# Kernel optimization log

Hardware: AMD Instinct MI355X
Metric: run time of the kernel (lower is better)

## Reference

```python
import jax, jax.numpy as jnp
import numpy as np

N_TOKEN = 267735
CUTOFFS = [20000, 40000, 200000, 267735]
ENDS = [0] + CUTOFFS
CLUSTER_DIMS = [1024, 256, 64, 16]   # d_embed // div_val**i
CLUSTER_SIZES = [20000, 20000, 160000, 67735]
D_PROJ = 1024
T, B = 256, 4
N_CLUSTERS = 3


def setup_inputs() -> dict:
    key = jax.random.key(0)
    ks = jax.random.split(key, 16)
    inp = {}
    inp["hidden"] = jax.random.normal(ks[0], (T, B, D_PROJ), jnp.float32)
    inp["target"] = jax.random.randint(ks[1], (T, B), 0, N_TOKEN)
    for i in range(4):
        inp[f"W{i}"] = jax.random.normal(ks[2 + 3 * i], (CLUSTER_SIZES[i], CLUSTER_DIMS[i]), jnp.float32) * 0.02
        inp[f"b{i}"] = jnp.zeros((CLUSTER_SIZES[i],), jnp.float32)
        inp[f"P{i}"] = jax.random.normal(ks[3 + 3 * i], (CLUSTER_DIMS[i], D_PROJ), jnp.float32) * 0.02
    inp["cluster_weight"] = jax.random.normal(ks[14], (N_CLUSTERS, 1024), jnp.float32) * 0.02
    inp["cluster_bias"] = jnp.zeros((N_CLUSTERS,), jnp.float32)
    return inp


def _logit(x, W, b, P):
    # x: [T,B,d_proj], P: [e,d_proj], W: [n,e] -> [T,B,n]
    y = jnp.einsum('ibd,ed->ibe', x, P)
    return jnp.einsum('ibe,ne->ibn', y, W) + b


def _gather(logprob, tgt):
    # pick logprob[t, b, tgt[t,b]]
    return jnp.take_along_axis(logprob, tgt[..., None], axis=-1)[..., 0]


def reference(hidden, target, W0, b0, P0, W1, b1, P1, W2, b2, P2, W3, b3, P3,
              cluster_weight, cluster_bias):
    Ws = [W0, W1, W2, W3]
    bs = [b0, b1, b2, b3]
    Ps = [P0, P1, P2, P3]
    loss = jnp.zeros(target.shape, jnp.float32)
    head_logprob = None
    for i in range(4):
        l_idx, r_idx = ENDS[i], ENDS[i + 1]
        mask = (target >= l_idx) & (target < r_idx)
        cur_t = jnp.maximum(jnp.minimum(target, r_idx - 1) - l_idx, 0)
        if i == 0:
            Wh = jnp.concatenate([W0, cluster_weight], axis=0)
            bh = jnp.concatenate([b0, cluster_bias], axis=0)
            head_logprob = jax.nn.log_softmax(_logit(hidden, Wh, bh, P0), axis=-1)
            cur_loss = _gather(head_logprob, cur_t)
        else:
            tail_logprob = jax.nn.log_softmax(_logit(hidden, Ws[i], bs[i], Ps[i]), axis=-1)
            logprob_i = head_logprob[..., CUTOFFS[0] + i - 1, None] + tail_logprob
            cur_loss = _gather(logprob_i, cur_t)
        loss = jnp.where(mask, cur_loss, loss)
    return jnp.mean(-loss)
```

## Files before the change

### kernel.cpp

```cpp
#include <hip/hip_runtime.h>
#include <math.h>

typedef short short8 __attribute__((ext_vector_type(8)));
typedef float f32x4 __attribute__((ext_vector_type(4)));
typedef unsigned long long u64;

#define LOG2E 1.4426950408889634f

__device__ __forceinline__ unsigned short f2bf_rne(float f) {
    unsigned u = __float_as_uint(f);
    unsigned r = (u + 0x7fff + ((u >> 16) & 1)) >> 16;
    return (unsigned short)r;
}
__device__ __forceinline__ float bf2f(unsigned short h) {
    return __uint_as_float(((unsigned)h) << 16);
}
__device__ __forceinline__ void load_lds16(const void* g, void* l) {
    __builtin_amdgcn_global_load_lds((const __attribute__((address_space(1))) void*)g,
                                     (__attribute__((address_space(3))) void*)l,
                                     16, 0, 0);
}
template<int N>
__device__ __forceinline__ void waitvm() {
    asm volatile("s_waitcnt vmcnt(%0)" :: "n"(N) : "memory");
}
__device__ __forceinline__ u64 pack8_fp8(const float* v, float s) {
    int lo = 0, hi = 0;
    lo = __builtin_amdgcn_cvt_pk_fp8_f32(v[0] * s, v[1] * s, lo, false);
    lo = __builtin_amdgcn_cvt_pk_fp8_f32(v[2] * s, v[3] * s, lo, true);
    hi = __builtin_amdgcn_cvt_pk_fp8_f32(v[4] * s, v[5] * s, hi, false);
    hi = __builtin_amdgcn_cvt_pk_fp8_f32(v[6] * s, v[7] * s, hi, true);
    return (u64)(unsigned)lo | ((u64)(unsigned)hi << 32);
}

__global__ void cvt_h(const float* __restrict__ in, unsigned short* __restrict__ out)
{
    const int i = blockIdx.x * 256 + threadIdx.x;
    const float4 v = *(const float4*)(in + (size_t)i * 4);
    ushort4 h;
    h.x = f2bf_rne(v.x); h.y = f2bf_rne(v.y);
    h.z = f2bf_rne(v.z); h.w = f2bf_rne(v.w);
    *(ushort4*)(out + (size_t)i * 4) = h;
}

struct ProjDesc {
    const float* B;
    unsigned short* Cbf;
    unsigned char* Cf8;
    int ldc; int nreal; int N; int Kpad; int gy_begin;
};

__global__ __launch_bounds__(256) void prepproj(
    const unsigned short* __restrict__ A,
    ProjDesc p0, ProjDesc p1, ProjDesc p2, ProjDesc p3,
    const float* __restrict__ W0, const float* __restrict__ cw,
    const float* __restrict__ W1, const float* __restrict__ W2,
    const float* __restrict__ W3,
    const float* __restrict__ b0, const float* __restrict__ cb,
    const float* __restrict__ b1, const float* __restrict__ b2,
    const float* __restrict__ b3,
    unsigned char* __restrict__ Wb0, unsigned char* __restrict__ Wb1,
    unsigned char* __restrict__ Wb2, unsigned char* __restrict__ Wb3,
    float* __restrict__ bp)
{
    __shared__ char smem[34816];

    const int tid = threadIdx.x;
    const int bx = blockIdx.x;

    if (bx >= 96) {
        const unsigned E0 = 1286144u;
        const unsigned E1 = 1613824u;
        const unsigned E2 = 2260992u;
        const unsigned E3 = 2539520u;
        const unsigned E4 = 2607520u;
        const unsigned stride = (gridDim.x - 96) * 256u;
        for (unsigned u = (bx - 96) * 256u + tid; u < E4; u += stride) {
            if (u < E3) {
                const float* src = nullptr;
                unsigned char* dstm; unsigned tile, kg2, r, tstride;
                if (u < E0) {
                    tile = u >> 13; const unsigned rem = u & 8191u;
                    kg2 = rem >> 7; r = rem & 127u;
                    const unsigned row = tile * 128u + r;
                    if (row < 20000u)      src = W0 + (size_t)row * 1024 + kg2 * 16;
                    else if (row < 20003u) src = cw + (size_t)(row - 20000u) * 1024 + kg2 * 16;
                    dstm = Wb0; tstride = 131072u;
                } else if (u < E1) {
                    const unsigned j = u - E0;
                    tile = j >> 11; const unsigned rem = j & 2047u;
                    kg2 = rem >> 7; r = rem & 127u;
                    const unsigned row = tile * 128u + r;
                    if (row < 20000u) src = W1 + (size_t)row * 256 + kg2 * 16;
                    dstm = Wb1; tstride = 32768u;
                } else if (u < E2) {
                    const unsigned j = u - E1;
                    tile = j >> 9; kg2 = (j >> 7) & 3u; r = j & 127u;
                    const unsigned row = tile * 128u + r;
                    if (row < 160000u) src = W2 + (size_t)row * 64 + kg2 * 16;
                    dstm = Wb2; tstride = 8192u;
                } else {
                    const unsigned j = u - E2;
                    tile = j >> 9; kg2 = (j >> 7) & 3u; r = j & 127u;
                    const unsigned row = tile * 128u + r;
                    if (kg2 == 0 && row < 67735u) src = W3 + (size_t)row * 16;
                    dstm = Wb3; tstride = 8192u;
                }
                float f[16];
                if (src) {
#pragma unroll
                    for (int q = 0; q < 4; ++q) {
                        const float4 v = *(const float4*)(src + q * 4);
                        f[q * 4 + 0] = v.x; f[q * 4 + 1] = v.y;
                        f[q * 4 + 2] = v.z; f[q * 4 + 3] = v.w;
                    }
                } else {
#pragma unroll
                    for (int q = 0; q < 16; ++q) f[q] = 0.f;
                }
                u64* dst = (u64*)(dstm + (size_t)tile * tstride);
                dst[(2 * kg2) * 128 + r]     = pack8_fp8(f,     16.0f);
                dst[(2 * kg2 + 1) * 128 + r] = pack8_fp8(f + 8, 16.0f);
            } else {
                const unsigned idx0 = (u - E3) * 4u;
                float e[4];
#pragma unroll
                for (int j = 0; j < 4; ++j) {
                    const unsigned idx = idx0 + j;
                    float v;
                    if (idx < 20096u) {
                        v = (idx < 20000u) ? b0[idx] * LOG2E
                          : (idx < 20003u) ? cb[idx - 20000u] * LOG2E : -1e30f;
                    } else if (idx < 40576u) {
                        const unsigned i1 = idx - 20096u;
                        v = (i1 < 20000u) ? b1[i1] * LOG2E : -1e30f;
                    } else if (idx < 202368u) {
                        const unsigned i2 = idx - 40576u;
                        v = (i2 < 160000u) ? b2[i2] * LOG2E : -1e30f;
                    } else {
                        const unsigned i3 = idx - 202368u;
                        v = (i3 < 67735u) ? b3[i3] * LOG2E : -1e30f;
                    }
                    e[j] = v;
                }
                *(float4*)(bp + idx0) = make_float4(e[0], e[1], e[2], e[3]);
            }
        }
        return;
    }

    unsigned short* As = (unsigned short*)smem;
    unsigned short* Bs = (unsigned short*)(smem + 16384);

    const int mt = bx & 7;
    const int py = bx >> 3;
    ProjDesc p = (py >= p3.gy_begin) ? p3 : (py >= p2.gy_begin) ? p2
               : (py >= p1.gy_begin) ? p1 : p0;

    const int w = tid >> 6;
    const int l = tid & 63;
    const int m0 = mt * 128;
    const int n0 = (py - p.gy_begin) * 128;
    const int wm = (w >> 1) * 64;
    const int wn = (w & 1) * 64;
    const int lane16 = l & 15;
    const int quad = l >> 4;

    const unsigned short* aptr[4];
    int ag_base[4];
#pragma unroll
    for (int i = 0; i < 4; ++i) {
        const int g = w * 256 + i * 64 + l;
        aptr[i] = A + (size_t)(m0 + (g & 127)) * 1024 + (g >> 7) * 8;
        ag_base[i] = (w * 256 + i * 64) * 8;
    }

    const int bn = tid >> 1;
    const int bhalf = tid & 1;
    int brow = n0 + bn;
    if (brow > p.N - 1) brow = p.N - 1;
    const float* brow_ptr = p.B + (size_t)brow * 1024;

    f32x4 acc[4][4] = {};

    for (int k0 = 0; k0 < 1024; k0 += 64) {
        __syncthreads();
#pragma unroll
        for (int i = 0; i < 4; ++i)
            load_lds16(aptr[i] + k0, (void*)&As[ag_base[i]]);
#pragma unroll
        for (int j = 0; j < 8; ++j) {
            const int kq = bhalf * 8 + j;
            const float4 v = *(const float4*)(brow_ptr + k0 + kq * 4);
            const unsigned px = __builtin_amdgcn_perm(__float_as_uint(v.y), __float_as_uint(v.x), 0x07060302);
            const unsigned pyv = __builtin_amdgcn_perm(__float_as_uint(v.w), __float_as_uint(v.z), 0x07060302);
            const int gran = (kq >> 1) * 128 + bn;
            *(uint2*)&Bs[gran * 8 + (kq & 1) * 4] = make_uint2(px, pyv);
        }
        __syncthreads();

#pragma unroll
        for (int kk = 0; kk < 2; ++kk) {
            const int kgb = kk * 4 + quad;
            short8 af[4], bfr[4];
#pragma unroll
            for (int mi = 0; mi < 4; ++mi)
                af[mi] = *(const short8*)&As[(kgb * 128 + wm + mi * 16 + lane16) * 8];
#pragma unroll
            for (int ni = 0; ni < 4; ++ni)
                bfr[ni] = *(const short8*)&Bs[(kgb * 128 + wn + ni * 16 + lane16) * 8];
#pragma unroll
            for (int mi = 0; mi < 4; ++mi)
#pragma unroll
                for (int ni = 0; ni < 4; ++ni)
                    acc[mi][ni] = __builtin_amdgcn_mfma_f32_16x16x32_bf16(
                        af[mi], bfr[ni], acc[mi][ni], 0, 0, 0);
        }
    }

#pragma unroll
    for (int mi = 0; mi < 4; ++mi)
#pragma unroll
        for (int ni = 0; ni < 4; ++ni) {
            const int n = n0 + wn + ni * 16 + lane16;
            if (n < p.ldc) {
#pragma unroll
                for (int r = 0; r < 4; ++r) {
                    const int m = m0 + wm + mi * 16 + quad * 4 + r;
                    const float v = (n < p.nreal) ? acc[mi][ni][r] : 0.f;
                    p.Cbf[(size_t)m * p.ldc + n] = f2bf_rne(v);
                }
            }
        }

    float* bounce = (float*)smem;
    u64* Yout = (u64*)p.Cf8 + (size_t)mt * 16 * p.Kpad;
    for (int c = 0; c < 2; ++c) {
        const int colbase = n0 + c * 64;
        if (colbase >= p.Kpad) break;
        __syncthreads();
        if ((w & 1) == c) {
#pragma unroll
            for (int mi = 0; mi < 4; ++mi)
#pragma unroll
                for (int ni = 0; ni < 4; ++ni) {
                    const int ncol = ni * 16 + lane16;
                    const bool real = (colbase + ncol) < p.nreal;
#pragma unroll
                    for (int r = 0; r < 4; ++r) {
                        const int m = wm + mi * 16 + quad * 4 + r;
                        bounce[m * 66 + ncol] = real ? acc[mi][ni][r] : 0.f;
                    }
                }
        }
        __syncthreads();
#pragma unroll
        for (int i = 0; i < 4; ++i) {
            const int g = i * 256 + tid;
            const int kgl = g >> 7;
            const int m = g & 127;
            float v[8];
#pragma unroll
            for (int j = 0; j < 8; ++j) v[j] = bounce[m * 66 + kgl * 8 + j];
            Yout[((colbase >> 3) + kgl) * 128 + m] = pack8_fp8(v, 4.0f);
        }
    }
}

struct ExpDesc {
    const unsigned char* A;
    const unsigned char* W;
    const float* bias;
    float* part;
    int Kpad; int ksl; int kmask; int gy_begin; int slab;
};

__global__ __launch_bounds__(512) void exp_gemm(ExpDesc d0, ExpDesc d1, ExpDesc d2, ExpDesc d3)
{
    __shared__ u64 As[2][2048];
    __shared__ u64 Bs[2][1024];
    __shared__ float biasLds[2][128];

    const int p = blockIdx.x;
    const int gy = blockIdx.y;

    ExpDesc d = (gy >= d3.gy_begin) ? d3 : (gy >= d2.gy_begin) ? d2
              : (gy >= d1.gy_begin) ? d1 : d0;

    const int tid = threadIdx.x;
    const int w = tid >> 6;
    const int l = tid & 63;
    const int wmt = w >> 2;
    const int wq = w & 3;
    const int wm = (wq >> 1) * 64;
    const int wn = (wq & 1) * 64;
    const int lane16 = l & 15;
    const int quad = l >> 4;

    const int tiles_begin = (gy - d.gy_begin) * d.slab;
    const int T = d.slab << d.ksl;
    const int kmask = d.kmask;
    const int ksl = d.ksl;
    const bool haveA = (kmask != 0);

    const size_t tstride = (size_t)128 * d.Kpad;
    const unsigned char* Abase0 = d.A + (size_t)p * tstride;
    const unsigned char* Abase1 = d.A + (size_t)(p + 4) * tstride;
    const unsigned char* Bbase = d.W + (size_t)tiles_begin * tstride;
    const float* biasBase = d.bias + (size_t)tiles_begin * 128;

    const int so = tid * 16;
    const int bu = (w * 4 + l) * 16;

    if (haveA) {
        load_lds16(Abase0 + so, (char*)As[0] + so);
        load_lds16(Abase1 + so, (char*)As[0] + 8192 + so);
        load_lds16(Bbase + so, (char*)Bs[0] + so);
        if (l < 4) load_lds16(biasBase + (bu >> 2), (char*)biasLds + bu);
        load_lds16(Abase0 + 8192 + so, (char*)As[1] + so);
        load_lds16(Abase1 + 8192 + so, (char*)As[1] + 8192 + so);
        load_lds16(Bbase + 8192 + so, (char*)Bs[1] + so);
        if (l < 4) load_lds16(biasBase + (bu >> 2), (char*)biasLds + 512 + bu);
    } else {
        load_lds16(Abase0 + so, (char*)As[0] + so);
        load_lds16(Abase1 + so, (char*)As[0] + 8192 + so);
        load_lds16(Bbase + so, (char*)Bs[0] + so);
        if (l < 4) load_lds16(biasBase + (bu >> 2), (char*)biasLds + bu);
        load_lds16(Bbase + tstride + so, (char*)Bs[1] + so);
        if (l < 4) load_lds16(biasBase + 128 + (bu >> 2), (char*)biasLds + 512 + bu);
    }

    f32x4 acc[4][4] = {};
    float rowsum[4][4] = {};
    const float c1 = LOG2E / 64.0f;

    for (int it = 0; it < T; ++it) {
        const int slot = it & 1;
        if (it + 1 < T) { if (haveA) waitvm<4>(); else waitvm<2>(); }
        else            { waitvm<0>(); }
        __builtin_amdgcn_s_barrier();
        __builtin_amdgcn_sched_barrier(0);

        const u64* Ar = (haveA ? As[slot] : As[0]) + wmt * 1024;
        const u64* Br = Bs[slot];
#pragma unroll
        for (int ks = 0; ks < 2; ++ks) {
            u64 af[4], bfr[4];
#pragma unroll
            for (int mi = 0; mi < 4; ++mi)
                af[mi] = Ar[(ks * 4 + quad) * 128 + wm + mi * 16 + lane16];
#pragma unroll
            for (int ni = 0; ni < 4; ++ni)
                bfr[ni] = Br[(ks * 4 + quad) * 128 + wn + ni * 16 + lane16];
#pragma unroll
            for (int mi = 0; mi < 4; ++mi)
#pragma unroll
                for (int ni = 0; ni < 4; ++ni)
                    acc[mi][ni] = __builtin_amdgcn_mfma_f32_16x16x32_fp8_fp8(
                        (long)af[mi], (long)bfr[ni], acc[mi][ni], 0, 0, 0);
        }

        const bool doflush = ((it & kmask) == kmask);
        float biasc[4];
        if (doflush) {
#pragma unroll
            for (int ni = 0; ni < 4; ++ni)
                biasc[ni] = biasLds[slot][wn + ni * 16 + lane16];
            asm volatile("s_waitcnt lgkmcnt(0)" ::: "memory");
        }

        __builtin_amdgcn_sched_barrier(0);
        __builtin_amdgcn_s_barrier();

        if (it + 2 < T) {
            const int nit = it + 2;
            const int kc = nit & kmask;
            const int tile = nit >> ksl;
            if (haveA) {
                load_lds16(Abase0 + kc * 8192 + so, (char*)As[slot] + so);
                load_lds16(Abase1 + kc * 8192 + so, (char*)As[slot] + 8192 + so);
            }
            const unsigned char* bc = Bbase + (size_t)tile * tstride + kc * 8192;
            load_lds16(bc + so, (char*)Bs[slot] + so);
            if (l < 4)
                load_lds16(biasBase + (size_t)tile * 128 + (bu >> 2),
                           (char*)biasLds + slot * 512 + bu);
        }

        if (doflush) {
#pragma unroll
            for (int mi = 0; mi < 4; ++mi)
#pragma unroll
                for (int r = 0; r < 4; ++r) {
                    float s = exp2f(fmaf(acc[mi][0][r], c1, biasc[0]))
                            + exp2f(fmaf(acc[mi][1][r], c1, biasc[1]))
                            + exp2f(fmaf(acc[mi][2][r], c1, biasc[2]))
                            + exp2f(fmaf(acc[mi][3][r], c1, biasc[3]));
                    rowsum[mi][r] += s;
                }
#pragma unroll
            for (int mi = 0; mi < 4; ++mi)
#pragma unroll
                for (int ni = 0; ni < 4; ++ni)
                    acc[mi][ni] = (f32x4){0.f, 0.f, 0.f, 0.f};
        }
    }

#pragma unroll
    for (int off = 1; off < 16; off <<= 1)
#pragma unroll
        for (int mi = 0; mi < 4; ++mi)
#pragma unroll
            for (int r = 0; r < 4; ++r)
                rowsum[mi][r] += __shfl_xor(rowsum[mi][r], off, 64);

    __syncthreads();
    float* buf = (float*)As;
    if (lane16 == 0) {
#pragma unroll
        for (int mi = 0; mi < 4; ++mi)
#pragma unroll
            for (int r = 0; r < 4; ++r)
                buf[(wmt * 128 + wm + mi * 16 + quad * 4 + r) * 2 + (wn >> 6)] = rowsum[mi][r];
    }
    __syncthreads();
    if (tid < 256) {
        const int row = tid & 127;
        const int mtreal = p + (tid >> 7) * 4;
        d.part[(size_t)(gy - d.gy_begin) * 1024 + mtreal * 128 + row] =
            buf[tid * 2 + 0] + buf[tid * 2 + 1];
    }
}

__global__ void redext(const float* __restrict__ p0, const float* __restrict__ p1,
                       const float* __restrict__ p2, const float* __restrict__ p3,
                       float* __restrict__ S,
                       const unsigned short* __restrict__ Y0, const unsigned short* __restrict__ Y1,
                       const unsigned short* __restrict__ Y2, const unsigned short* __restrict__ Y3,
                       const int* __restrict__ target,
                       const float* __restrict__ W0, const float* __restrict__ b0,
                       const float* __restrict__ W1, const float* __restrict__ b1,
                       const float* __restrict__ W2, const float* __restrict__ b2,
                       const float* __restrict__ W3, const float* __restrict__ b3,
                       const float* __restrict__ cw, const float* __restrict__ cb,
                       float* __restrict__ headlogit, float* __restrict__ taillogit)
{
    if (blockIdx.x < 16) {
        const int idx = blockIdx.x * 256 + threadIdx.x;
        const int c = idx >> 10, m = idx & 1023;
        const float* p = (c == 0) ? p0 : (c == 1) ? p1 : (c == 2) ? p2 : p3;
        const int G = (c == 0) ? 157 : (c == 1) ? 40 : (c == 2) ? 79 : 34;
        float s = 0.f;
        for (int y = 0; y < G; ++y) s += p[(size_t)y * 1024 + m];
        S[idx] = s;
        return;
    }
    const int token = (blockIdx.x - 16) * 4 + (threadIdx.x >> 6);
    const int lane = threadIdx.x & 63;
    const int tgt = target[token];
    const int ci = (tgt < 20000) ? 0 : (tgt < 40000) ? 1 : (tgt < 200000) ? 2 : 3;

    {
        const int h = (ci == 0) ? tgt : (20000 + ci - 1);
        const float* row;
        float bb;
        if (h < 20000) { row = W0 + (size_t)h * 1024; bb = b0[h]; }
        else           { row = cw + (size_t)(h - 20000) * 1024; bb = cb[h - 20000]; }
        const unsigned short* y = Y0 + (size_t)token * 1024;
        float s = 0.f;
        for (int k = lane; k < 1024; k += 64) s += bf2f(y[k]) * row[k];
#pragma unroll
        for (int off = 1; off < 64; off <<= 1) s += __shfl_xor(s, off, 64);
        if (lane == 0) headlogit[token] = s + bb;
    }

    float tl = 0.f;
    if (ci > 0) {
        const unsigned short* Y; const float* W; const float* b; int K, ldy, lidx;
        if (ci == 1)      { Y = Y1; W = W1; b = b1; K = 256; ldy = 256; lidx = 20000; }
        else if (ci == 2) { Y = Y2; W = W2; b = b2; K = 64;  ldy = 64;  lidx = 40000; }
        else              { Y = Y3; W = W3; b = b3; K = 16;  ldy = 64;  lidx = 200000; }
        const int r = tgt - lidx;
        const unsigned short* y = Y + (size_t)token * ldy;
        const float* row = W + (size_t)r * K;
        float s = 0.f;
        for (int k = lane; k < K; k += 64) s += bf2f(y[k]) * row[k];
#pragma unroll
        for (int off = 1; off < 64; off <<= 1) s += __shfl_xor(s, off, 64);
        tl = s + b[r];
    }
    if (lane == 0) taillogit[token] = tl;
}

__global__ void finalize_kernel(const float* __restrict__ S,
                                const int* __restrict__ target,
                                const float* __restrict__ headlogit,
                                const float* __restrict__ taillogit,
                                float* __restrict__ out)
{
    __shared__ float red[256];
    const int tid = threadIdx.x;
    float acc = 0.f;
    for (int token = tid; token < 1024; token += 256) {
        const int tgt = target[token];
        const int ci = (tgt < 20000) ? 0 : (tgt < 40000) ? 1 : (tgt < 200000) ? 2 : 3;
        float lp = headlogit[token] - logf(S[token]);
        if (ci > 0)
            lp += taillogit[token] - logf(S[ci * 1024 + token]);
        acc -= lp;
    }
    red[tid] = acc;
    __syncthreads();
    for (int s = 128; s > 0; s >>= 1) {
        if (tid < s) red[tid] += red[tid + s];
        __syncthreads();
    }
    if (tid == 0) out[0] = red[0] * (1.0f / 1024.0f);
}

extern "C" void kernel_launch(void* const* d_in, const int* in_sizes, int n_in,
                              void* d_out, int out_size, void* d_ws, size_t ws_size,
                              hipStream_t stream)
{
    const float* hidden = (const float*)d_in[0];
    const int*   target = (const int*)d_in[1];
    const float* W0 = (const float*)d_in[2];  const float* b0 = (const float*)d_in[3];  const float* P0 = (const float*)d_in[4];
    const float* W1 = (const float*)d_in[5];  const float* b1 = (const float*)d_in[6];  const float* P1 = (const float*)d_in[7];
    const float* W2 = (const float*)d_in[8];  const float* b2 = (const float*)d_in[9];  const float* P2 = (const float*)d_in[10];
    const float* W3 = (const float*)d_in[11]; const float* b3 = (const float*)d_in[12]; const float* P3 = (const float*)d_in[13];
    const float* cw = (const float*)d_in[14]; const float* cb = (const float*)d_in[15];
    float* out = (float*)d_out;

    unsigned char* ws = (unsigned char*)d_ws;
    unsigned short* h_bf = (unsigned short*)ws;
    unsigned short* Y0bf = (unsigned short*)(ws + 2097152);
    unsigned short* Y1bf = (unsigned short*)(ws + 4194304);
    unsigned short* Y2bf = (unsigned short*)(ws + 4718592);
    unsigned short* Y3bf = (unsigned short*)(ws + 4849664);
    unsigned char* Y0f8 = ws + 4980736;
    unsigned char* Y1f8 = ws + 6029312;
    unsigned char* Y2f8 = ws + 6291456;
    unsigned char* Y3f8 = ws + 6356992;
    unsigned char* Wb0 = ws + 6422528;
    unsigned char* Wb1 = ws + 27000832;
    unsigned char* Wb2 = ws + 32243712;
    unsigned char* Wb3 = ws + 42598400;
    float* bp = (float*)(ws + 47054848);

    float* part0 = (float*)ws;
    float* part1 = part0 + (size_t)157 * 1024;
    float* part2 = part1 + (size_t)40 * 1024;
    float* part3 = part2 + (size_t)79 * 1024;
    float* S = part3 + (size_t)34 * 1024;
    float* headlogit = S + 4096;
    float* taillogit = headlogit + 1024;

    cvt_h<<<1024, 256, 0, stream>>>(hidden, h_bf);

    ProjDesc pr0 = { P0, Y0bf, Y0f8, 1024, 1024, 1024, 1024, 0 };
    ProjDesc pr1 = { P1, Y1bf, Y1f8, 256,  256,  256,  256,  8 };
    ProjDesc pr2 = { P2, Y2bf, Y2f8, 64,   64,   64,   64,   10 };
    ProjDesc pr3 = { P3, Y3bf, Y3f8, 64,   16,   16,   64,   11 };
    prepproj<<<2048, 256, 0, stream>>>(h_bf, pr0, pr1, pr2, pr3,
                                       W0, cw, W1, W2, W3,
                                       b0, cb, b1, b2, b3,
                                       Wb0, Wb1, Wb2, Wb3, bp);

    ExpDesc d0 = { Y0f8, Wb0, bp,          part0, 1024, 4, 15, 0,   1 };
    ExpDesc d1 = { Y1f8, Wb1, bp + 20096,  part1, 256,  2, 3,  157, 4 };
    ExpDesc d2 = { Y2f8, Wb2, bp + 40576,  part2, 64,   0, 0,  197, 16 };
    ExpDesc d3 = { Y3f8, Wb3, bp + 202368, part3, 64,   0, 0,  276, 16 };
    exp_gemm<<<dim3(4, 310), 512, 0, stream>>>(d0, d1, d2, d3);

    redext<<<272, 256, 0, stream>>>(part0, part1, part2, part3, S,
                                    Y0bf, Y1bf, Y2bf, Y3bf, target,
                                    W0, b0, W1, b1, W2, b2, W3, b3,
                                    cw, cb, headlogit, taillogit);

    finalize_kernel<<<1, 256, 0, stream>>>(S, target, headlogit, taillogit, out);
}
```

Measured before the change: 396.2 us.

## Stage fp8 weight conversion through LDS for coalesced reads and writes

```diff
diff --git a/kernel.cpp b/kernel.cpp
--- a/kernel.cpp
+++ b/kernel.cpp
@@ -69,82 +69,142 @@
     const int bx = blockIdx.x;
 
     if (bx >= 96) {
-        const unsigned E0 = 1286144u;
-        const unsigned E1 = 1613824u;
-        const unsigned E2 = 2260992u;
-        const unsigned E3 = 2539520u;
-        const unsigned E4 = 2607520u;
+        u64* lds = (u64*)smem;
+        const int NP = 2596;
+        const int nconv = gridDim.x - 96;
+        for (int pn = bx - 96; pn < NP; pn += nconv) {
+            __syncthreads();
+            if (pn < 788) {
+                const bool isW0 = (pn < 628);
+                const int tile = isW0 ? (pn >> 2) : (pn - 628);
+                const int c0 = isW0 ? (pn & 3) * 256 : 0;
+                unsigned char* dstm = isW0 ? Wb0 : Wb1;
+                const int tstride = isW0 ? 131072 : 32768;
+#pragma unroll
+                for (int rp = 0; rp < 8; ++rp) {
+                    const int row = rp * 16 + (tid >> 4);
+                    const int colf = (tid & 15) * 16;
+                    const int row_g = tile * 128 + row;
+                    const float* s = nullptr;
+                    if (isW0) {
+                        if (row_g < 20000)      s = W0 + (size_t)row_g * 1024 + c0 + colf;
+                        else if (row_g < 20003) s = cw + (size_t)(row_g - 20000) * 1024 + c0 + colf;
+                    } else {
+                        if (row_g < 20000)      s = W1 + (size_t)row_g * 256 + colf;
+                    }
+                    float f[16];
+                    if (s) {
+#pragma unroll
+                        for (int q = 0; q < 4; ++q) {
+                            const float4 v = *(const float4*)(s + q * 4);
+                            f[q * 4 + 0] = v.x; f[q * 4 + 1] = v.y;
+                            f[q * 4 + 2] = v.z; f[q * 4 + 3] = v.w;
+                        }
+                    } else {
+#pragma unroll
+                        for (int q = 0; q < 16; ++q) f[q] = 0.f;
+                    }
+                    const int kg = (tid & 15) * 2;
+                    lds[kg * 130 + row]       = pack8_fp8(f,     16.0f);
+                    lds[(kg + 1) * 130 + row] = pack8_fp8(f + 8, 16.0f);
+                }
+                __syncthreads();
+                u64* dst = (u64*)(dstm + (size_t)tile * tstride) + (size_t)(c0 >> 3) * 128;
+#pragma unroll
+                for (int i = 0; i < 16; ++i) {
+                    const int lin = i * 256 + tid;
+                    const int kg = lin >> 7, r = lin & 127;
+                    dst[lin] = lds[kg * 130 + r];
+                }
+            } else if (pn < 2052) {
+                const int tile = pn - 788;
+#pragma unroll
+                for (int rp = 0; rp < 2; ++rp) {
+                    const int row = rp * 64 + (tid >> 2);
+                    const int colf = (tid & 3) * 16;
+                    const int row_g = tile * 128 + row;
+                    const float* s = (row_g < 160000) ? W2 + (size_t)row_g * 64 + colf : nullptr;
+                    float f[16];
+                    if (s) {
+#pragma unroll
+                        for (int q = 0; q < 4; ++q) {
+                            const float4 v = *(const float4*)(s + q * 4);
+                            f[q * 4 + 0] = v.x; f[q * 4 + 1] = v.y;
+                            f[q * 4 + 2] = v.z; f[q * 4 + 3] = v.w;
+                        }
+                    } else {
+#pragma unroll
+                        for (int q = 0; q < 16; ++q) f[q] = 0.f;
+                    }
+                    const int kg = (tid & 3) * 2;
+                    lds[kg * 130 + row]       = pack8_fp8(f,     16.0f);
+                    lds[(kg + 1) * 130 + row] = pack8_fp8(f + 8, 16.0f);
+                }
+                __syncthreads();
+                u64* dst = (u64*)(Wb2 + (size_t)tile * 8192);
+#pragma unroll
+                for (int i = 0; i < 4; ++i) {
+                    const int lin = i * 256 + tid;
+                    const int kg = lin >> 7, r = lin & 127;
+                    dst[lin] = lds[kg * 130 + r];
+                }
+            } else {
+                const int tile = pn - 2052;
+                if (tid < 128) {
+                    const int row = tid;
+                    const int row_g = tile * 128 + row;
+                    const float* s = (row_g < 67735) ? W3 + (size_t)row_g * 16 : nullptr;
+                    float f[16];
+                    if (s) {
+#pragma unroll
+                        for (int q = 0; q < 4; ++q) {
+                            const float4 v = *(const float4*)(s + q * 4);
+                            f[q * 4 + 0] = v.x; f[q * 4 + 1] = v.y;
+                            f[q * 4 + 2] = v.z; f[q * 4 + 3] = v.w;
+                        }
+                    } else {
+#pragma unroll
+                        for (int q = 0; q < 16; ++q) f[q] = 0.f;
+                    }
+                    lds[row]       = pack8_fp8(f,     16.0f);
+                    lds[130 + row] = pack8_fp8(f + 8, 16.0f);
+                }
+                __syncthreads();
+                u64* dst = (u64*)(Wb3 + (size_t)tile * 8192);
+#pragma unroll
+                for (int i = 0; i < 4; ++i) {
+                    const int lin = i * 256 + tid;
+                    const int kg = lin >> 7, r = lin & 127;
+                    dst[lin] = (kg < 2) ? lds[kg * 130 + r] : 0ull;
+                }
+            }
+        }
+
+        const unsigned BN = 68000u;
         const unsigned stride = (gridDim.x - 96) * 256u;
-        for (unsigned u = (bx - 96) * 256u + tid; u < E4; u += stride) {
-            if (u < E3) {
-                const float* src = nullptr;
-                unsigned char* dstm; unsigned tile, kg2, r, tstride;
-                if (u < E0) {
-                    tile = u >> 13; const unsigned rem = u & 8191u;
-                    kg2 = rem >> 7; r = rem & 127u;
-                    const unsigned row = tile * 128u + r;
-                    if (row < 20000u)      src = W0 + (size_t)row * 1024 + kg2 * 16;
-                    else if (row < 20003u) src = cw + (size_t)(row - 20000u) * 1024 + kg2 * 16;
-                    dstm = Wb0; tstride = 131072u;
-                } else if (u < E1) {
-                    const unsigned j = u - E0;
-                    tile = j >> 11; const unsigned rem = j & 2047u;
-                    kg2 = rem >> 7; r = rem & 127u;
-                    const unsigned row = tile * 128u + r;
-                    if (row < 20000u) src = W1 + (size_t)row * 256 + kg2 * 16;
-                    dstm = Wb1; tstride = 32768u;
-                } else if (u < E2) {
-                    const unsigned j = u - E1;
-                    tile = j >> 9; kg2 = (j >> 7) & 3u; r = j & 127u;
-                    const unsigned row = tile * 128u + r;
-                    if (row < 160000u) src = W2 + (size_t)row * 64 + kg2 * 16;
-                    dstm = Wb2; tstride = 8192u;
+        for (unsigned u = (bx - 96) * 256u + tid; u < BN; u += stride) {
+            const unsigned idx0 = u * 4u;
+            float e[4];
+#pragma unroll
+            for (int j = 0; j < 4; ++j) {
+                const unsigned idx = idx0 + j;
+                float v;
+                if (idx < 20096u) {
+                    v = (idx < 20000u) ? b0[idx] * LOG2E
+                      : (idx < 20003u) ? cb[idx - 20000u] * LOG2E : -1e30f;
+                } else if (idx < 40576u) {
+                    const unsigned i1 = idx - 20096u;
+                    v = (i1 < 20000u) ? b1[i1] * LOG2E : -1e30f;
+                } else if (idx < 202368u) {
+                    const unsigned i2 = idx - 40576u;
+                    v = (i2 < 160000u) ? b2[i2] * LOG2E : -1e30f;
                 } else {
-                    const unsigned j = u - E2;
-                    tile = j >> 9; kg2 = (j >> 7) & 3u; r = j & 127u;
-                    const unsigned row = tile * 128u + r;
-                    if (kg2 == 0 && row < 67735u) src = W3 + (size_t)row * 16;
-                    dstm = Wb3; tstride = 8192u;
-                }
-                float f[16];
-                if (src) {
-#pragma unroll
-                    for (int q = 0; q < 4; ++q) {
-                        const float4 v = *(const float4*)(src + q * 4);
-                        f[q * 4 + 0] = v.x; f[q * 4 + 1] = v.y;
-                        f[q * 4 + 2] = v.z; f[q * 4 + 3] = v.w;
-                    }
-                } else {
-#pragma unroll
-                    for (int q = 0; q < 16; ++q) f[q] = 0.f;
-                }
-                u64* dst = (u64*)(dstm + (size_t)tile * tstride);
-                dst[(2 * kg2) * 128 + r]     = pack8_fp8(f,     16.0f);
-                dst[(2 * kg2 + 1) * 128 + r] = pack8_fp8(f + 8, 16.0f);
-            } else {
-                const unsigned idx0 = (u - E3) * 4u;
-                float e[4];
-#pragma unroll
-                for (int j = 0; j < 4; ++j) {
-                    const unsigned idx = idx0 + j;
-                    float v;
-                    if (idx < 20096u) {
-                        v = (idx < 20000u) ? b0[idx] * LOG2E
-                          : (idx < 20003u) ? cb[idx - 20000u] * LOG2E : -1e30f;
-                    } else if (idx < 40576u) {
-                        const unsigned i1 = idx - 20096u;
-                        v = (i1 < 20000u) ? b1[i1] * LOG2E : -1e30f;
-                    } else if (idx < 202368u) {
-                        const unsigned i2 = idx - 40576u;
-                        v = (i2 < 160000u) ? b2[i2] * LOG2E : -1e30f;
-                    } else {
-                        const unsigned i3 = idx - 202368u;
-                        v = (i3 < 67735u) ? b3[i3] * LOG2E : -1e30f;
-                    }
-                    e[j] = v;
-                }
-                *(float4*)(bp + idx0) = make_float4(e[0], e[1], e[2], e[3]);
+                    const unsigned i3 = idx - 202368u;
+                    v = (i3 < 67735u) ? b3[i3] * LOG2E : -1e30f;
+                }
+                e[j] = v;
             }
+            *(float4*)(bp + idx0) = make_float4(e[0], e[1], e[2], e[3]);
         }
         return;
     }
```

Result: no change. 391.0 us (-1.3%).
